# Kernel tuning notes

Measured on AMD Instinct MI355X. Metric: run time of the kernel, lower is better.

## Reference

```python
import jax, jax.numpy as jnp
import numpy as np

EMBED_DIM = 512
FFN_DIM = 2048
N_QUBITS = 8
BATCH = 16
SEQ = 2048


def setup_inputs() -> dict:
    key = jax.random.key(0)
    k_x, k_t, k_w1, k_w2 = jax.random.split(key, 4)
    x = jax.random.normal(k_x, (BATCH, SEQ, EMBED_DIM), dtype=jnp.float32)
    # per-wire trainable RX angles (nn.Parameter(torch.randn(1)) per qubit)
    theta = jax.random.normal(k_t, (N_QUBITS,), dtype=jnp.float32)
    # nn.Linear weights, bias=False; stored as [out, in] like torch
    s1 = 1.0 / np.sqrt(N_QUBITS)
    s2 = 1.0 / np.sqrt(FFN_DIM)
    W1 = jax.random.uniform(k_w1, (FFN_DIM, N_QUBITS), jnp.float32, -s1, s1)
    W2 = jax.random.uniform(k_w2, (EMBED_DIM, FFN_DIM), jnp.float32, -s2, s2)
    return {"x": x, "theta": theta, "W1": W1, "W2": W2}


def reference(x, theta, W1, W2):
    # Quantum circuit closed form: each wire i gets RX(x_i) twice (outer loop
    # + encoder) plus trainable RX(theta_i); product state => <Z_i> = cos(total angle).
    q = jnp.cos(2.0 * x[..., :N_QUBITS] + theta)          # [B, S, n_qubits]
    # dropout in eval mode is identity
    h = jax.nn.relu(jnp.einsum('bsq,fq->bsf', q, W1))     # [B, S, ffn_dim]
    out = jnp.einsum('bsf,ef->bse', h, W2)                # [B, S, embed_dim]
    return out
```

## Files before the change

### kernel.cpp

```cpp
#include <hip/hip_runtime.h>
#include <cstdint>

#define BATCH 16
#define SEQ 2048
#define EMB 512
#define FFN 2048
#define NQ 8
#define M_TOTAL (BATCH * SEQ)

#define BM 128
#define BN 256
#define BK 32
#define NTHREADS 512

typedef __attribute__((ext_vector_type(8))) short short8;
typedef __attribute__((ext_vector_type(4))) float float4v;
typedef __attribute__((ext_vector_type(4))) unsigned int uint4v;

static __device__ __forceinline__ unsigned int f2bf(float f) {
    unsigned int u = __builtin_bit_cast(unsigned int, f);
    return (u + 0x7fffu + ((u >> 16) & 1u)) >> 16;
}
static __device__ __forceinline__ unsigned int f2bf_pk(float lo, float hi) {
    return f2bf(lo) | (f2bf(hi) << 16);
}
static __device__ __forceinline__ unsigned int cvt_pk_bf16(float lo, float hi) {
    unsigned int r;
    asm("v_cvt_pk_bf16_f32 %0, %1, %2" : "=v"(r) : "v"(lo), "v"(hi));
    return r;
}

__global__ __launch_bounds__(256) void prep_w2(const float* __restrict__ W2,
                                               unsigned int* __restrict__ w2b) {
    int idx = (blockIdx.x * 256 + threadIdx.x) * 4;
    float4 v = *(const float4*)&W2[idx];
    w2b[idx / 2]     = f2bf_pk(v.x, v.y);
    w2b[idx / 2 + 1] = f2bf_pk(v.z, v.w);
}


__global__ __launch_bounds__(NTHREADS, 4) void ffq_main(
    const float* __restrict__ x,
    const float* __restrict__ theta,
    const unsigned short* __restrict__ w1b,
    const unsigned short* __restrict__ w2b,
    float* __restrict__ out)
{
    __shared__ unsigned short Asm[2][BM * BK];
    __shared__ unsigned short Bsm[2][BN * BK];

    const int t    = threadIdx.x;
    const int m0   = blockIdx.x * BM;
    const int n0   = blockIdx.y * BN;
    const int wave = t >> 6, lane = t & 63;
    const int quad = lane >> 4, l16 = lane & 15;
    const int wm   = wave >> 2, wn = wave & 3;

    short8 qfrag;
    {
        int qrow = m0 + wave * 16 + l16;
        const float* xr = x + (size_t)qrow * EMB;
        float4 xa = *(const float4*)xr;
        float4 xb = *(const float4*)(xr + 4);
        uint4v uq;
        uq[0] = f2bf_pk(__cosf(2.f * xa.x + theta[0]), __cosf(2.f * xa.y + theta[1]));
        uq[1] = f2bf_pk(__cosf(2.f * xa.z + theta[2]), __cosf(2.f * xa.w + theta[3]));
        uq[2] = f2bf_pk(__cosf(2.f * xb.x + theta[4]), __cosf(2.f * xb.y + theta[5]));
        uq[3] = f2bf_pk(__cosf(2.f * xb.z + theta[6]), __cosf(2.f * xb.w + theta[7]));
        qfrag = __builtin_bit_cast(short8, uq);
        if (quad != 0) qfrag = (short8)0;
    }

    const int c0 = t, c1 = NTHREADS + t;
    const int n0c0 = c0 >> 2, s0c = c0 & 3;
    const int n0c1 = c1 >> 2, s1c = c1 & 3;
    const unsigned short* gB0 =
        w2b + (size_t)(n0 + n0c0) * FFN + (s0c ^ ((n0c0 >> 1) & 3)) * 8;
    const unsigned short* gB1 =
        w2b + (size_t)(n0 + n0c1) * FFN + (s1c ^ ((n0c1 >> 1) & 3)) * 8;

    auto stageB = [&](int k0, int buf) __attribute__((always_inline)) {
        __builtin_amdgcn_global_load_lds(
            (const __attribute__((address_space(1))) unsigned int*)(gB0 + k0),
            (__attribute__((address_space(3))) unsigned int*)(uintptr_t)(&Bsm[buf][c0 * 8]),
            16, 0, 0);
        __builtin_amdgcn_global_load_lds(
            (const __attribute__((address_space(1))) unsigned int*)(gB1 + k0),
            (__attribute__((address_space(3))) unsigned int*)(uintptr_t)(&Bsm[buf][c1 * 8]),
            16, 0, 0);
    };

    auto loadW1 = [&](int kh, short8& a, short8& b) __attribute__((always_inline)) {
        a = *(const short8*)&w1b[(size_t)(kh + l16) * NQ];
        b = *(const short8*)&w1b[(size_t)(kh + 16 + l16) * NQ];
    };

    const int hswz = (l16 >> 1) & 3;
    const int hm   = wave * 16 + l16;
    auto hgen = [&](int buf, short8 w1f0, short8 w1f1) __attribute__((always_inline)) {
#pragma unroll
        for (int fh = 0; fh < 2; ++fh) {
            float4v hc = __builtin_amdgcn_mfma_f32_16x16x32_bf16(
                fh ? w1f1 : w1f0, qfrag, (float4v)0.0f, 0, 0, 0);
            unsigned int p0 = cvt_pk_bf16(fmaxf(hc[0], 0.f), fmaxf(hc[1], 0.f));
            unsigned int p1 = cvt_pk_bf16(fmaxf(hc[2], 0.f), fmaxf(hc[3], 0.f));
            int qph = (fh * 2 + (quad >> 1)) ^ hswz;
            unsigned long long pk = ((unsigned long long)p1 << 32) | p0;
            *(unsigned long long*)&Asm[buf][hm * 32 + qph * 8 + (quad & 1) * 4] = pk;
        }
    };

    float4v acc[16];
#pragma unroll
    for (int i = 0; i < 16; ++i) acc[i] = (float4v)0.0f;

    auto compute = [&](int buf) __attribute__((always_inline)) {
        short8 af[4], bfr[4];
#pragma unroll
        for (int fm = 0; fm < 4; ++fm) {
            int row = wm * 64 + fm * 16 + l16;
            int qph = quad ^ ((row >> 1) & 3);
            af[fm] = *(const short8*)&Asm[buf][row * 32 + qph * 8];
        }
#pragma unroll
        for (int fn = 0; fn < 4; ++fn) {
            int row = wn * 64 + fn * 16 + l16;
            int qph = quad ^ ((row >> 1) & 3);
            bfr[fn] = *(const short8*)&Bsm[buf][row * 32 + qph * 8];
        }
        __builtin_amdgcn_s_setprio(1);
#pragma unroll
        for (int fm = 0; fm < 4; ++fm)
#pragma unroll
            for (int fn = 0; fn < 4; ++fn)
                acc[fm * 4 + fn] = __builtin_amdgcn_mfma_f32_16x16x32_bf16(
                    af[fm], bfr[fn], acc[fm * 4 + fn], 0, 0, 0);
        __builtin_amdgcn_s_setprio(0);
    };

    {
        short8 w1f0, w1f1;
        loadW1(0, w1f0, w1f1);
        stageB(0, 0);
        hgen(0, w1f0, w1f1);
    }
    __syncthreads();

    for (int kt = 0; kt < 62; kt += 2) {
        {
            short8 w1f0, w1f1;
            loadW1((kt + 1) * BK, w1f0, w1f1);
            stageB((kt + 1) * BK, 1);
            compute(0);
            hgen(1, w1f0, w1f1);
        }
        __syncthreads();
        {
            short8 w1f0, w1f1;
            loadW1((kt + 2) * BK, w1f0, w1f1);
            stageB((kt + 2) * BK, 0);
            compute(1);
            hgen(0, w1f0, w1f1);
        }
        __syncthreads();
    }
    {
        short8 w1f0, w1f1;
        loadW1(63 * BK, w1f0, w1f1);
        stageB(63 * BK, 1);
        compute(0);
        hgen(1, w1f0, w1f1);
    }
    __syncthreads();
    compute(1);

    const int om = m0 + wm * 64;
    const int on = n0 + wn * 64;
#pragma unroll
    for (int fm = 0; fm < 4; ++fm) {
#pragma unroll
        for (int fn = 0; fn < 4; ++fn) {
            float4v v = acc[fm * 4 + fn];
            int rbase = om + fm * 16 + quad * 4;
            int c     = on + fn * 16 + l16;
#pragma unroll
            for (int r = 0; r < 4; ++r)
                out[(size_t)(rbase + r) * EMB + c] = v[r];
        }
    }
}

extern "C" void kernel_launch(void* const* d_in, const int* in_sizes, int n_in,
                              void* d_out, int out_size, void* d_ws, size_t ws_size,
                              hipStream_t stream) {
    const float* x     = (const float*)d_in[0];
    const float* theta = (const float*)d_in[1];
    const float* W1    = (const float*)d_in[2];
    const float* W2    = (const float*)d_in[3];
    float* out = (float*)d_out;

    unsigned int* w2b = (unsigned int*)d_ws;
    unsigned int* w1b = (unsigned int*)((char*)d_ws + (size_t)EMB * FFN * 2);

    prep_w2<<<(EMB * FFN) / (256 * 4), 256, 0, stream>>>(W2, w2b);
    prep_w2<<<(FFN * NQ) / (256 * 4), 256, 0, stream>>>(W1, w1b);

    dim3 grid(M_TOTAL / BM, EMB / BN);
    ffq_main<<<grid, NTHREADS, 0, stream>>>(x, theta,
                                            (const unsigned short*)w1b,
                                            (const unsigned short*)w2b, out);
}
```

Baseline: 176.5 us.

## Halve block to four waves with 64x128 per-wave output tiles

Cuts the workgroup from 8 waves to 4 and doubles each wave's output tile to 64x128, so each wave holds 32 accumulator fragments and reuses every A fragment across 8 B fragments. Each wave now generates hidden activations for two 16-row groups and issues four global-to-LDS loads per stage. The aim is less LDS read traffic per MFMA and lower per-thread index overhead. In exchange register pressure roughly doubles (128 accumulator VGPRs) and there are fewer waves to hide latency.

```diff
diff --git a/kernel.cpp b/kernel.cpp
--- a/kernel.cpp
+++ b/kernel.cpp
@@ -11,7 +11,7 @@
 #define BM 128
 #define BN 256
 #define BK 32
-#define NTHREADS 512
+#define NTHREADS 256
 
 typedef __attribute__((ext_vector_type(8))) short short8;
 typedef __attribute__((ext_vector_type(4))) float float4v;
@@ -39,7 +39,7 @@
 }
 
 
-__global__ __launch_bounds__(NTHREADS, 4) void ffq_main(
+__global__ __launch_bounds__(NTHREADS, 2) void ffq_main(
     const float* __restrict__ x,
     const float* __restrict__ theta,
     const unsigned short* __restrict__ w1b,
@@ -54,11 +54,12 @@
     const int n0   = blockIdx.y * BN;
     const int wave = t >> 6, lane = t & 63;
     const int quad = lane >> 4, l16 = lane & 15;
-    const int wm   = wave >> 2, wn = wave & 3;
-
-    short8 qfrag;
-    {
-        int qrow = m0 + wave * 16 + l16;
+    const int wm   = wave >> 1, wn = wave & 1;
+
+    short8 qfrag[2];
+#pragma unroll
+    for (int g2 = 0; g2 < 2; ++g2) {
+        int qrow = m0 + wave * 32 + g2 * 16 + l16;
         const float* xr = x + (size_t)qrow * EMB;
         float4 xa = *(const float4*)xr;
         float4 xb = *(const float4*)(xr + 4);
@@ -67,27 +68,27 @@
         uq[1] = f2bf_pk(__cosf(2.f * xa.z + theta[2]), __cosf(2.f * xa.w + theta[3]));
         uq[2] = f2bf_pk(__cosf(2.f * xb.x + theta[4]), __cosf(2.f * xb.y + theta[5]));
         uq[3] = f2bf_pk(__cosf(2.f * xb.z + theta[6]), __cosf(2.f * xb.w + theta[7]));
-        qfrag = __builtin_bit_cast(short8, uq);
-        if (quad != 0) qfrag = (short8)0;
-    }
-
-    const int c0 = t, c1 = NTHREADS + t;
-    const int n0c0 = c0 >> 2, s0c = c0 & 3;
-    const int n0c1 = c1 >> 2, s1c = c1 & 3;
-    const unsigned short* gB0 =
-        w2b + (size_t)(n0 + n0c0) * FFN + (s0c ^ ((n0c0 >> 1) & 3)) * 8;
-    const unsigned short* gB1 =
-        w2b + (size_t)(n0 + n0c1) * FFN + (s1c ^ ((n0c1 >> 1) & 3)) * 8;
+        qfrag[g2] = __builtin_bit_cast(short8, uq);
+        if (quad != 0) qfrag[g2] = (short8)0;
+    }
+
+    const unsigned short* gB[4];
+#pragma unroll
+    for (int i = 0; i < 4; ++i) {
+        int c = i * NTHREADS + t;
+        int n = c >> 2, s = c & 3;
+        gB[i] = w2b + (size_t)(n0 + n) * FFN + (s ^ ((n >> 1) & 3)) * 8;
+    }
 
     auto stageB = [&](int k0, int buf) __attribute__((always_inline)) {
-        __builtin_amdgcn_global_load_lds(
-            (const __attribute__((address_space(1))) unsigned int*)(gB0 + k0),
-            (__attribute__((address_space(3))) unsigned int*)(uintptr_t)(&Bsm[buf][c0 * 8]),
-            16, 0, 0);
-        __builtin_amdgcn_global_load_lds(
-            (const __attribute__((address_space(1))) unsigned int*)(gB1 + k0),
-            (__attribute__((address_space(3))) unsigned int*)(uintptr_t)(&Bsm[buf][c1 * 8]),
-            16, 0, 0);
+#pragma unroll
+        for (int i = 0; i < 4; ++i) {
+            int c = i * NTHREADS + t;
+            __builtin_amdgcn_global_load_lds(
+                (const __attribute__((address_space(1))) unsigned int*)(gB[i] + k0),
+                (__attribute__((address_space(3))) unsigned int*)(uintptr_t)(&Bsm[buf][c * 8]),
+                16, 0, 0);
+        }
     };
 
     auto loadW1 = [&](int kh, short8& a, short8& b) __attribute__((always_inline)) {
@@ -96,26 +97,29 @@
     };
 
     const int hswz = (l16 >> 1) & 3;
-    const int hm   = wave * 16 + l16;
     auto hgen = [&](int buf, short8 w1f0, short8 w1f1) __attribute__((always_inline)) {
 #pragma unroll
-        for (int fh = 0; fh < 2; ++fh) {
-            float4v hc = __builtin_amdgcn_mfma_f32_16x16x32_bf16(
-                fh ? w1f1 : w1f0, qfrag, (float4v)0.0f, 0, 0, 0);
-            unsigned int p0 = cvt_pk_bf16(fmaxf(hc[0], 0.f), fmaxf(hc[1], 0.f));
-            unsigned int p1 = cvt_pk_bf16(fmaxf(hc[2], 0.f), fmaxf(hc[3], 0.f));
-            int qph = (fh * 2 + (quad >> 1)) ^ hswz;
-            unsigned long long pk = ((unsigned long long)p1 << 32) | p0;
-            *(unsigned long long*)&Asm[buf][hm * 32 + qph * 8 + (quad & 1) * 4] = pk;
-        }
-    };
-
-    float4v acc[16];
-#pragma unroll
-    for (int i = 0; i < 16; ++i) acc[i] = (float4v)0.0f;
+        for (int g2 = 0; g2 < 2; ++g2) {
+#pragma unroll
+            for (int fh = 0; fh < 2; ++fh) {
+                float4v hc = __builtin_amdgcn_mfma_f32_16x16x32_bf16(
+                    fh ? w1f1 : w1f0, qfrag[g2], (float4v)0.0f, 0, 0, 0);
+                unsigned int p0 = cvt_pk_bf16(fmaxf(hc[0], 0.f), fmaxf(hc[1], 0.f));
+                unsigned int p1 = cvt_pk_bf16(fmaxf(hc[2], 0.f), fmaxf(hc[3], 0.f));
+                int m   = wave * 32 + g2 * 16 + l16;
+                int qph = (fh * 2 + (quad >> 1)) ^ hswz;
+                unsigned long long pk = ((unsigned long long)p1 << 32) | p0;
+                *(unsigned long long*)&Asm[buf][m * 32 + qph * 8 + (quad & 1) * 4] = pk;
+            }
+        }
+    };
+
+    float4v acc[32];
+#pragma unroll
+    for (int i = 0; i < 32; ++i) acc[i] = (float4v)0.0f;
 
     auto compute = [&](int buf) __attribute__((always_inline)) {
-        short8 af[4], bfr[4];
+        short8 af[4], bfr[8];
 #pragma unroll
         for (int fm = 0; fm < 4; ++fm) {
             int row = wm * 64 + fm * 16 + l16;
@@ -123,8 +127,8 @@
             af[fm] = *(const short8*)&Asm[buf][row * 32 + qph * 8];
         }
 #pragma unroll
-        for (int fn = 0; fn < 4; ++fn) {
-            int row = wn * 64 + fn * 16 + l16;
+        for (int fn = 0; fn < 8; ++fn) {
+            int row = wn * 128 + fn * 16 + l16;
             int qph = quad ^ ((row >> 1) & 3);
             bfr[fn] = *(const short8*)&Bsm[buf][row * 32 + qph * 8];
         }
@@ -132,9 +136,9 @@
 #pragma unroll
         for (int fm = 0; fm < 4; ++fm)
 #pragma unroll
-            for (int fn = 0; fn < 4; ++fn)
-                acc[fm * 4 + fn] = __builtin_amdgcn_mfma_f32_16x16x32_bf16(
-                    af[fm], bfr[fn], acc[fm * 4 + fn], 0, 0, 0);
+            for (int fn = 0; fn < 8; ++fn)
+                acc[fm * 8 + fn] = __builtin_amdgcn_mfma_f32_16x16x32_bf16(
+                    af[fm], bfr[fn], acc[fm * 8 + fn], 0, 0, 0);
         __builtin_amdgcn_s_setprio(0);
     };
 
@@ -175,12 +179,12 @@
     compute(1);
 
     const int om = m0 + wm * 64;
-    const int on = n0 + wn * 64;
+    const int on = n0 + wn * 128;
 #pragma unroll
     for (int fm = 0; fm < 4; ++fm) {
 #pragma unroll
-        for (int fn = 0; fn < 4; ++fn) {
-            float4v v = acc[fm * 4 + fn];
+        for (int fn = 0; fn < 8; ++fn) {
+            float4v v = acc[fm * 8 + fn];
             int rbase = om + fm * 16 + quad * 4;
             int c     = on + fn * 16 + l16;
 #pragma unroll
```

After: 173.4 us. No clear change (-1.8%).
